# Kernel tuning notes

Measured on AMD Instinct MI355X. Metric: run time of the kernel, lower is better.

Reference implementation:

```python
import jax, jax.numpy as jnp
import numpy as np

N_NODES = 50000
N_EDGES = 1600000
NUM_GRAPHS = 64


def gcn_conv(x, edge_index, edge_weight, W, b):
    # PyG GCNConv with normalize=False: h = x @ W; out[i] = sum_{e: tgt(e)=i} w_e * h[src(e)]; out += b
    h = x @ W                                   # [N, out]
    src, tgt = edge_index[0], edge_index[1]
    msg = h[src] * edge_weight[:, None]         # [E, out] gather + scale
    out = jax.ops.segment_sum(msg, tgt, num_segments=N_NODES)
    return out + b


def setup_inputs() -> dict:
    key = jax.random.key(0)
    ks = jax.random.split(key, 10)
    x = jax.random.normal(ks[0], (N_NODES, 128), dtype=jnp.float32)
    edge_index = jax.random.randint(ks[1], (2, N_EDGES), 0, N_NODES, dtype=jnp.int64)
    edge_weight = jax.random.uniform(ks[2], (N_EDGES,), dtype=jnp.float32)
    batch = jnp.sort(jax.random.randint(ks[3], (N_NODES,), 0, NUM_GRAPHS, dtype=jnp.int64))
    W1 = jax.random.normal(ks[4], (128, 64), dtype=jnp.float32) * 0.09  # ~glorot scale
    b1 = jax.random.normal(ks[5], (64,), dtype=jnp.float32) * 0.01
    W2 = jax.random.normal(ks[6], (64, 64), dtype=jnp.float32) * 0.125
    b2 = jax.random.normal(ks[7], (64,), dtype=jnp.float32) * 0.01
    W3 = jax.random.normal(ks[8], (64, 64), dtype=jnp.float32) * 0.125
    b3 = jax.random.normal(ks[9], (64,), dtype=jnp.float32) * 0.01
    return {"x": x, "edge_index": edge_index, "edge_weight": edge_weight, "batch": batch,
            "W1": W1, "b1": b1, "W2": W2, "b2": b2, "W3": W3, "b3": b3}


def reference(x, edge_index, edge_weight, batch, W1, b1, W2, b2, W3, b3):
    # dropout is identity in eval mode
    h = jax.nn.relu(gcn_conv(x, edge_index, edge_weight, W1, b1))
    embed = gcn_conv(h, edge_index, edge_weight, W2, b2)
    graph = gcn_conv(h, edge_index, edge_weight, W3, b3)
    graph_embed = jax.ops.segment_sum(graph, batch, num_segments=NUM_GRAPHS)
    return (embed, graph_embed)
```

## Files before the change

### kernel.cpp

```cpp
#include <hip/hip_runtime.h>


typedef _Float16 f16;
typedef _Float16 h2v __attribute__((ext_vector_type(2)));

#define THREADS 256
#define BTHREADS 1024
#define NODECAP 80
#define NC 391
#define CSTRIDE 16
#define ACH 4096
#define CAPC 4736

__global__ __launch_bounds__(BTHREADS) void bin_coarse(
    const int* __restrict__ src, const int* __restrict__ tgt,
    const float* __restrict__ ew, int* __restrict__ cnt_a,
    int2* __restrict__ cbins, int E) {
  __shared__ int lcnt[NC];
  __shared__ int gbase[NC];
  int tid = threadIdx.x;
  for (int i = tid; i < NC; i += BTHREADS) lcnt[i] = 0;
  __syncthreads();

  int e0 = blockIdx.x * ACH;
  int xr[4], wr[4], cr[4];
#pragma unroll
  for (int k = 0; k < 4; ++k) {
    int e = e0 + k * BTHREADS + tid;
    if (e < E) {
      int t = tgt[e];
      int c = t >> 7;
      int r = atomicAdd(&lcnt[c], 1);
      xr[k] = (src[e] & 0xffff) | ((t & 127) << 16);
      wr[k] = __float_as_int(ew[e]);
      cr[k] = c | (r << 16);
    } else {
      cr[k] = -1;
    }
  }
  __syncthreads();

  for (int c = tid; c < NC; c += BTHREADS) {
    int n = lcnt[c];
    gbase[c] = n ? atomicAdd(&cnt_a[c * CSTRIDE], n) : 0;
  }
  __syncthreads();

#pragma unroll
  for (int k = 0; k < 4; ++k) {
    if (cr[k] < 0) continue;
    int c = cr[k] & 0xffff;
    int r = cr[k] >> 16;
    int dst = gbase[c] + r;
    if (dst < CAPC) cbins[(size_t)c * CAPC + dst] = make_int2(xr[k], wr[k]);
  }
}

__global__ __launch_bounds__(BTHREADS) void bin_fine(
    const int* __restrict__ cnt_a, const int2* __restrict__ cbins,
    int* __restrict__ cnt_f, int2* __restrict__ fbins, int N) {
  __shared__ int fcnt[128];
  int c = blockIdx.x;
  int tid = threadIdx.x;
  if (tid < 128) fcnt[tid] = 0;
  __syncthreads();
  int d = min(cnt_a[c * CSTRIDE], CAPC);
  const int2* ep = cbins + (size_t)c * CAPC;
  for (int i = tid; i < d; i += BTHREADS) {
    int2 ent = ep[i];
    int tl = ent.x >> 16;
    int r = atomicAdd(&fcnt[tl], 1);
    int node = c * 128 + tl;
    if (r < NODECAP && node < N)
      fbins[(size_t)node * NODECAP + r] = make_int2((ent.x & 0xffff) << 7, ent.y);
  }
  __syncthreads();
  if (tid < 128) {
    int node = c * 128 + tid;
    if (node < N) cnt_f[node] = min(fcnt[tid], NODECAP);
  }
}

template <bool RELU>
__global__ __launch_bounds__(THREADS) void gather_nodes(
    const f16* __restrict__ h, const int2* __restrict__ fbins,
    const int* __restrict__ cnt, const float* __restrict__ bias,
    f16* __restrict__ out, int N) {
  int tid = threadIdx.x;
  int lane = tid & 63;
  int node = blockIdx.x * 4 + (tid >> 6);
  if (node >= N) return;
  int d = min(cnt[node], NODECAP);
  const int2* ep = fbins + (size_t)node * NODECAP;
  const char* hb = (const char*)h;
  int q = lane >> 4;
  int lq = lane & 15;
  int lq8 = lq * 8;
  float4 acc = make_float4(0.f, 0.f, 0.f, 0.f);

  for (int base = 0; base < d; base += 64) {
    int take = min(64, d - base);
    int2 ent = ep[base + min(lane, take - 1)];
    int pv = ent.x;
    float wv = (lane < take) ? __int_as_float(ent.y) : 0.f;

    for (int g0 = 0; g0 < take; g0 += 32) {
      int off[8]; float w[8];
#pragma unroll
      for (int u = 0; u < 8; ++u) {
        int sl = g0 + u * 4 + q;
        off[u] = __shfl(pv, sl, 64);
        w[u]   = __shfl(wv, sl, 64);
      }
      uint2 r8[8];
#pragma unroll
      for (int u = 0; u < 8; ++u)
        r8[u] = *(const uint2*)(hb + off[u] + lq8);
#pragma unroll
      for (int u = 0; u < 8; ++u) {
        h2v p0 = __builtin_bit_cast(h2v, r8[u].x);
        h2v p1 = __builtin_bit_cast(h2v, r8[u].y);
        acc.x = fmaf((float)p0.x, w[u], acc.x);
        acc.y = fmaf((float)p0.y, w[u], acc.y);
        acc.z = fmaf((float)p1.x, w[u], acc.z);
        acc.w = fmaf((float)p1.y, w[u], acc.w);
      }
    }
  }

  acc.x += __shfl_xor(acc.x, 16, 64); acc.x += __shfl_xor(acc.x, 32, 64);
  acc.y += __shfl_xor(acc.y, 16, 64); acc.y += __shfl_xor(acc.y, 32, 64);
  acc.z += __shfl_xor(acc.z, 16, 64); acc.z += __shfl_xor(acc.z, 32, 64);
  acc.w += __shfl_xor(acc.w, 16, 64); acc.w += __shfl_xor(acc.w, 32, 64);

  if (q == 0) {
    union { f16 h4[4]; uint2 u; } pk;
    if (RELU) {
      float4 bb = *(const float4*)(bias + lq * 4);
      pk.h4[0] = (f16)fmaxf(acc.x + bb.x, 0.f);
      pk.h4[1] = (f16)fmaxf(acc.y + bb.y, 0.f);
      pk.h4[2] = (f16)fmaxf(acc.z + bb.z, 0.f);
      pk.h4[3] = (f16)fmaxf(acc.w + bb.w, 0.f);
    } else {
      pk.h4[0] = (f16)acc.x; pk.h4[1] = (f16)acc.y;
      pk.h4[2] = (f16)acc.z; pk.h4[3] = (f16)acc.w;
    }
    *(uint2*)((char*)out + (size_t)node * 128 + lq8) = pk.u;
  }
}

template <int K, bool BIAS, typename InT, typename OutT>
__global__ __launch_bounds__(THREADS) void gemm_tiled(
    const InT* __restrict__ A, const float* __restrict__ W,
    const float* __restrict__ bias, OutT* __restrict__ C, int M) {
  __shared__ float Xs[K][68];
  __shared__ float Ws[K][64];
  int tid = threadIdx.x;
  int r0 = blockIdx.x * 64;

  for (int i = tid * 4; i < K * 64; i += THREADS * 4)
    *(float4*)&Ws[0][i] = *(const float4*)(W + i);

  constexpr int KSH = (K == 128) ? 7 : 6;
  for (int i = tid * 4; i < 64 * K; i += THREADS * 4) {
    int row = i >> KSH, k = i & (K - 1);
    float4 v = make_float4(0.f, 0.f, 0.f, 0.f);
    if (r0 + row < M) {
      if constexpr (sizeof(InT) == 2) {
        uint2 u = *(const uint2*)((const f16*)A + (size_t)(r0 + row) * K + k);
        h2v a0 = __builtin_bit_cast(h2v, u.x);
        h2v a1 = __builtin_bit_cast(h2v, u.y);
        v = make_float4((float)a0.x, (float)a0.y, (float)a1.x, (float)a1.y);
      } else {
        v = *(const float4*)((const float*)A + (size_t)(r0 + row) * K + k);
      }
    }
    Xs[k + 0][row] = v.x; Xs[k + 1][row] = v.y;
    Xs[k + 2][row] = v.z; Xs[k + 3][row] = v.w;
  }
  __syncthreads();

  int tx = tid & 15, ty = tid >> 4;
  float acc[4][4] = {};
#pragma unroll 8
  for (int k = 0; k < K; ++k) {
    float4 w4 = *(const float4*)&Ws[k][tx * 4];
    float4 x4 = *(const float4*)&Xs[k][ty * 4];
    acc[0][0] = fmaf(x4.x, w4.x, acc[0][0]); acc[0][1] = fmaf(x4.x, w4.y, acc[0][1]);
    acc[0][2] = fmaf(x4.x, w4.z, acc[0][2]); acc[0][3] = fmaf(x4.x, w4.w, acc[0][3]);
    acc[1][0] = fmaf(x4.y, w4.x, acc[1][0]); acc[1][1] = fmaf(x4.y, w4.y, acc[1][1]);
    acc[1][2] = fmaf(x4.y, w4.z, acc[1][2]); acc[1][3] = fmaf(x4.y, w4.w, acc[1][3]);
    acc[2][0] = fmaf(x4.z, w4.x, acc[2][0]); acc[2][1] = fmaf(x4.z, w4.y, acc[2][1]);
    acc[2][2] = fmaf(x4.z, w4.z, acc[2][2]); acc[2][3] = fmaf(x4.z, w4.w, acc[2][3]);
    acc[3][0] = fmaf(x4.w, w4.x, acc[3][0]); acc[3][1] = fmaf(x4.w, w4.y, acc[3][1]);
    acc[3][2] = fmaf(x4.w, w4.z, acc[3][2]); acc[3][3] = fmaf(x4.w, w4.w, acc[3][3]);
  }
#pragma unroll
  for (int i = 0; i < 4; ++i) {
    int r = r0 + ty * 4 + i;
    if (r >= M) continue;
    float4 o = make_float4(acc[i][0], acc[i][1], acc[i][2], acc[i][3]);
    if (BIAS) {
      float4 bb = *(const float4*)(bias + tx * 4);
      o.x += bb.x; o.y += bb.y; o.z += bb.z; o.w += bb.w;
    }
    if constexpr (sizeof(OutT) == 2) {
      union { f16 h4[4]; uint2 u; } pk;
      pk.h4[0] = (f16)o.x; pk.h4[1] = (f16)o.y;
      pk.h4[2] = (f16)o.z; pk.h4[3] = (f16)o.w;
      *(uint2*)((f16*)C + (size_t)r * 64 + tx * 4) = pk.u;
    } else {
      *(float4*)((float*)C + (size_t)r * 64 + tx * 4) = o;
    }
  }
}

__global__ __launch_bounds__(THREADS) void graph_reduce(
    const f16* __restrict__ A, const int* __restrict__ batch,
    float* __restrict__ B, float* __restrict__ counts, int N) {
  int lane = threadIdx.x & 63;
  int chunk = blockIdx.x * (THREADS >> 6) + (threadIdx.x >> 6);
  int n0 = chunk * 64;
  if (n0 >= N) return;
  int n1 = min(n0 + 64, N);
  int cur = batch[n0];
  float acc = 0.f, cnt = 0.f;
  for (int n = n0; n < n1; ++n) {
    int g = batch[n];
    if (g != cur) {
      unsafeAtomicAdd(&B[cur * 64 + lane], acc);
      if (lane == 0) unsafeAtomicAdd(&counts[cur], cnt);
      acc = 0.f; cnt = 0.f; cur = g;
    }
    acc += (float)A[(size_t)n * 64 + lane];
    cnt += 1.f;
  }
  unsafeAtomicAdd(&B[cur * 64 + lane], acc);
  if (lane == 0) unsafeAtomicAdd(&counts[cur], cnt);
}

__global__ __launch_bounds__(THREADS) void graph_out_k(
    const float* __restrict__ B, const float* __restrict__ W3,
    const float* __restrict__ b3, const float* __restrict__ counts,
    float* __restrict__ out, int G) {
  int j = threadIdx.x & 63;
  int g = blockIdx.x * (THREADS >> 6) + (threadIdx.x >> 6);
  if (g >= G) return;
  float acc = 0.f;
#pragma unroll
  for (int k = 0; k < 64; ++k) acc += B[g * 64 + k] * W3[k * 64 + j];
  out[g * 64 + j] = acc + counts[g] * b3[j];
}

extern "C" void kernel_launch(void* const* d_in, const int* in_sizes, int n_in,
                              void* d_out, int out_size, void* d_ws, size_t ws_size,
                              hipStream_t stream) {
  const float* x     = (const float*)d_in[0];
  const int*   ei    = (const int*)d_in[1];
  const float* ew    = (const float*)d_in[2];
  const int*   batch = (const int*)d_in[3];
  const float* W1    = (const float*)d_in[4];
  const float* b1    = (const float*)d_in[5];
  const float* W2    = (const float*)d_in[6];
  const float* b2    = (const float*)d_in[7];
  const float* W3    = (const float*)d_in[8];
  const float* b3    = (const float*)d_in[9];

  const int N = in_sizes[0] / 128;
  const int E = in_sizes[1] / 2;
  const int G = (out_size - N * 64) / 64;
  const int* src = ei;
  const int* tgt = ei + E;

  float* out_embed = (float*)d_out;
  float* out_graph = (float*)d_out + (size_t)N * 64;

  char* ws = (char*)d_ws;
  f16*   hpre   = (f16*)ws;
  f16*   h1     = (f16*)(ws + (size_t)N * 64 * 2);
  f16*   A      = (f16*)(ws + (size_t)N * 64 * 4);
  int2*  cbins  = (int2*)ws;
  int*   cnt_f  = (int*)(ws + (size_t)N * 64 * 8);
  int*   cnt_a  = cnt_f + N;
  float* B      = (float*)(cnt_a + NC * CSTRIDE);
  float* counts = B + (size_t)G * 64;
  size_t meta_bytes = (size_t)(N + NC * CSTRIDE) * 4 + (size_t)(G * 64 + G) * 4;
  size_t base   = (size_t)N * 64 * 8 + meta_bytes;
  size_t fin_off = (base + 255) & ~(size_t)255;
  int2*  fbins  = (int2*)(ws + fin_off);

  hipMemsetAsync(cnt_f, 0, meta_bytes, stream);

  bin_coarse<<<(E + ACH - 1) / ACH, BTHREADS, 0, stream>>>(
      src, tgt, ew, cnt_a, cbins, E);
  bin_fine<<<NC, BTHREADS, 0, stream>>>(cnt_a, cbins, cnt_f, fbins, N);

  gemm_tiled<128, false, float, f16><<<(N + 63) / 64, THREADS, 0, stream>>>(
      x, W1, nullptr, hpre, N);

  const int gblocks = (N + 3) / 4;
  gather_nodes<true><<<gblocks, THREADS, 0, stream>>>(
      hpre, fbins, cnt_f, b1, h1, N);
  gather_nodes<false><<<gblocks, THREADS, 0, stream>>>(
      h1, fbins, cnt_f, nullptr, A, N);

  gemm_tiled<64, true, f16, float><<<(N + 63) / 64, THREADS, 0, stream>>>(
      A, W2, b2, out_embed, N);

  int chunks = (N + 63) / 64;
  graph_reduce<<<(chunks + 3) / 4, THREADS, 0, stream>>>(A, batch, B, counts, N);

  graph_out_k<<<(G + 3) / 4, THREADS, 0, stream>>>(B, W3, b3, counts, out_graph, G);
}
```

Before: 245.6 us.

## Co-schedule coarse binning with first GEMM and fuse graph reduce into second GEMM

```diff
diff --git a/kernel.cpp b/kernel.cpp
--- a/kernel.cpp
+++ b/kernel.cpp
@@ -12,21 +12,23 @@
 #define ACH 4096
 #define CAPC 4736
 
-__global__ __launch_bounds__(BTHREADS) void bin_coarse(
-    const int* __restrict__ src, const int* __restrict__ tgt,
-    const float* __restrict__ ew, int* __restrict__ cnt_a,
-    int2* __restrict__ cbins, int E) {
-  __shared__ int lcnt[NC];
-  __shared__ int gbase[NC];
-  int tid = threadIdx.x;
-  for (int i = tid; i < NC; i += BTHREADS) lcnt[i] = 0;
-  __syncthreads();
-
-  int e0 = blockIdx.x * ACH;
-  int xr[4], wr[4], cr[4];
-#pragma unroll
-  for (int k = 0; k < 4; ++k) {
-    int e = e0 + k * BTHREADS + tid;
+#define SMEM_BYTES (128 * 68 * 4 + 128 * 64 * 4)
+
+__device__ __forceinline__ void bin_coarse_body(
+    int bid, char* smem, const int* __restrict__ src,
+    const int* __restrict__ tgt, const float* __restrict__ ew,
+    int* __restrict__ cnt_a, int2* __restrict__ cbins, int E) {
+  int* lcnt  = (int*)smem;
+  int* gbase = lcnt + NC;
+  int tid = threadIdx.x;
+  for (int i = tid; i < NC; i += THREADS) lcnt[i] = 0;
+  __syncthreads();
+
+  int e0 = bid * ACH;
+  int xr[16], wr[16], cr[16];
+#pragma unroll
+  for (int k = 0; k < 16; ++k) {
+    int e = e0 + k * THREADS + tid;
     if (e < E) {
       int t = tgt[e];
       int c = t >> 7;
@@ -40,19 +42,83 @@
   }
   __syncthreads();
 
-  for (int c = tid; c < NC; c += BTHREADS) {
+  for (int c = tid; c < NC; c += THREADS) {
     int n = lcnt[c];
     gbase[c] = n ? atomicAdd(&cnt_a[c * CSTRIDE], n) : 0;
   }
   __syncthreads();
 
 #pragma unroll
-  for (int k = 0; k < 4; ++k) {
+  for (int k = 0; k < 16; ++k) {
     if (cr[k] < 0) continue;
     int c = cr[k] & 0xffff;
     int r = cr[k] >> 16;
     int dst = gbase[c] + r;
     if (dst < CAPC) cbins[(size_t)c * CAPC + dst] = make_int2(xr[k], wr[k]);
+  }
+}
+
+__device__ __forceinline__ void gemm1_body(
+    int bid, char* smem, const float* __restrict__ A,
+    const float* __restrict__ W, f16* __restrict__ C, int M) {
+  float (*Xs)[68] = (float(*)[68])smem;
+  float (*Ws)[64] = (float(*)[64])(smem + 128 * 68 * 4);
+  int tid = threadIdx.x;
+  int r0 = bid * 64;
+
+  for (int i = tid * 4; i < 128 * 64; i += THREADS * 4)
+    *(float4*)&Ws[0][i] = *(const float4*)(W + i);
+
+  for (int i = tid * 4; i < 64 * 128; i += THREADS * 4) {
+    int row = i >> 7, k = i & 127;
+    float4 v = make_float4(0.f, 0.f, 0.f, 0.f);
+    if (r0 + row < M) v = *(const float4*)(A + (size_t)(r0 + row) * 128 + k);
+    Xs[k + 0][row] = v.x; Xs[k + 1][row] = v.y;
+    Xs[k + 2][row] = v.z; Xs[k + 3][row] = v.w;
+  }
+  __syncthreads();
+
+  int tx = tid & 15, ty = tid >> 4;
+  float acc[4][4] = {};
+#pragma unroll 8
+  for (int k = 0; k < 128; ++k) {
+    float4 w4 = *(const float4*)&Ws[k][tx * 4];
+    float4 x4 = *(const float4*)&Xs[k][ty * 4];
+    acc[0][0] = fmaf(x4.x, w4.x, acc[0][0]); acc[0][1] = fmaf(x4.x, w4.y, acc[0][1]);
+    acc[0][2] = fmaf(x4.x, w4.z, acc[0][2]); acc[0][3] = fmaf(x4.x, w4.w, acc[0][3]);
+    acc[1][0] = fmaf(x4.y, w4.x, acc[1][0]); acc[1][1] = fmaf(x4.y, w4.y, acc[1][1]);
+    acc[1][2] = fmaf(x4.y, w4.z, acc[1][2]); acc[1][3] = fmaf(x4.y, w4.w, acc[1][3]);
+    acc[2][0] = fmaf(x4.z, w4.x, acc[2][0]); acc[2][1] = fmaf(x4.z, w4.y, acc[2][1]);
+    acc[2][2] = fmaf(x4.z, w4.z, acc[2][2]); acc[2][3] = fmaf(x4.z, w4.w, acc[2][3]);
+    acc[3][0] = fmaf(x4.w, w4.x, acc[3][0]); acc[3][1] = fmaf(x4.w, w4.y, acc[3][1]);
+    acc[3][2] = fmaf(x4.w, w4.z, acc[3][2]); acc[3][3] = fmaf(x4.w, w4.w, acc[3][3]);
+  }
+#pragma unroll
+  for (int i = 0; i < 4; ++i) {
+    int r = r0 + ty * 4 + i;
+    if (r >= M) continue;
+    union { f16 h4[4]; uint2 u; } pk;
+    pk.h4[0] = (f16)acc[i][0]; pk.h4[1] = (f16)acc[i][1];
+    pk.h4[2] = (f16)acc[i][2]; pk.h4[3] = (f16)acc[i][3];
+    *(uint2*)(C + (size_t)r * 64 + tx * 4) = pk.u;
+  }
+}
+
+__global__ __launch_bounds__(THREADS) void k_bin_gemm(
+    const int* __restrict__ src, const int* __restrict__ tgt,
+    const float* __restrict__ ew, int* __restrict__ cnt_a,
+    int2* __restrict__ cbins, int E,
+    const float* __restrict__ x, const float* __restrict__ W1,
+    f16* __restrict__ hpre, int M, int NBIN, int NGEMM) {
+  __shared__ __align__(16) char smem[SMEM_BYTES];
+  int b = blockIdx.x;
+  int binid = (b % 3 == 0) ? b / 3 : -1;
+  if (binid >= 0 && binid < NBIN) {
+    bin_coarse_body(binid, smem, src, tgt, ew, cnt_a, cbins, E);
+  } else {
+    int nb = min((b + 2) / 3, NBIN);
+    int gi = b - nb;
+    if (gi < NGEMM) gemm1_body(gi, smem, x, W1, hpre, M);
   }
 }
 
@@ -149,31 +215,29 @@
   }
 }
 
-template <int K, bool BIAS, typename InT, typename OutT>
-__global__ __launch_bounds__(THREADS) void gemm_tiled(
-    const InT* __restrict__ A, const float* __restrict__ W,
-    const float* __restrict__ bias, OutT* __restrict__ C, int M) {
-  __shared__ float Xs[K][68];
-  __shared__ float Ws[K][64];
+__global__ __launch_bounds__(THREADS) void k_gemm2_reduce(
+    const f16* __restrict__ A, const float* __restrict__ W,
+    const float* __restrict__ bias, const int* __restrict__ batch,
+    float* __restrict__ C, float* __restrict__ B, float* __restrict__ counts,
+    int M) {
+  __shared__ float Xs[64][68];
+  __shared__ float Ws[64][64];
+  __shared__ int bsh[64];
   int tid = threadIdx.x;
   int r0 = blockIdx.x * 64;
 
-  for (int i = tid * 4; i < K * 64; i += THREADS * 4)
+  for (int i = tid * 4; i < 64 * 64; i += THREADS * 4)
     *(float4*)&Ws[0][i] = *(const float4*)(W + i);
-
-  constexpr int KSH = (K == 128) ? 7 : 6;
-  for (int i = tid * 4; i < 64 * K; i += THREADS * 4) {
-    int row = i >> KSH, k = i & (K - 1);
+  if (tid < 64) bsh[tid] = (r0 + tid < M) ? batch[r0 + tid] : -1;
+
+  for (int i = tid * 4; i < 64 * 64; i += THREADS * 4) {
+    int row = i >> 6, k = i & 63;
     float4 v = make_float4(0.f, 0.f, 0.f, 0.f);
     if (r0 + row < M) {
-      if constexpr (sizeof(InT) == 2) {
-        uint2 u = *(const uint2*)((const f16*)A + (size_t)(r0 + row) * K + k);
-        h2v a0 = __builtin_bit_cast(h2v, u.x);
-        h2v a1 = __builtin_bit_cast(h2v, u.y);
-        v = make_float4((float)a0.x, (float)a0.y, (float)a1.x, (float)a1.y);
-      } else {
-        v = *(const float4*)((const float*)A + (size_t)(r0 + row) * K + k);
-      }
+      uint2 u = *(const uint2*)(A + (size_t)(r0 + row) * 64 + k);
+      h2v a0 = __builtin_bit_cast(h2v, u.x);
+      h2v a1 = __builtin_bit_cast(h2v, u.y);
+      v = make_float4((float)a0.x, (float)a0.y, (float)a1.x, (float)a1.y);
     }
     Xs[k + 0][row] = v.x; Xs[k + 1][row] = v.y;
     Xs[k + 2][row] = v.z; Xs[k + 3][row] = v.w;
@@ -183,7 +247,7 @@
   int tx = tid & 15, ty = tid >> 4;
   float acc[4][4] = {};
 #pragma unroll 8
-  for (int k = 0; k < K; ++k) {
+  for (int k = 0; k < 64; ++k) {
     float4 w4 = *(const float4*)&Ws[k][tx * 4];
     float4 x4 = *(const float4*)&Xs[k][ty * 4];
     acc[0][0] = fmaf(x4.x, w4.x, acc[0][0]); acc[0][1] = fmaf(x4.x, w4.y, acc[0][1]);
@@ -199,44 +263,34 @@
   for (int i = 0; i < 4; ++i) {
     int r = r0 + ty * 4 + i;
     if (r >= M) continue;
-    float4 o = make_float4(acc[i][0], acc[i][1], acc[i][2], acc[i][3]);
-    if (BIAS) {
-      float4 bb = *(const float4*)(bias + tx * 4);
-      o.x += bb.x; o.y += bb.y; o.z += bb.z; o.w += bb.w;
-    }
-    if constexpr (sizeof(OutT) == 2) {
-      union { f16 h4[4]; uint2 u; } pk;
-      pk.h4[0] = (f16)o.x; pk.h4[1] = (f16)o.y;
-      pk.h4[2] = (f16)o.z; pk.h4[3] = (f16)o.w;
-      *(uint2*)((f16*)C + (size_t)r * 64 + tx * 4) = pk.u;
-    } else {
-      *(float4*)((float*)C + (size_t)r * 64 + tx * 4) = o;
-    }
-  }
-}
-
-__global__ __launch_bounds__(THREADS) void graph_reduce(
-    const f16* __restrict__ A, const int* __restrict__ batch,
-    float* __restrict__ B, float* __restrict__ counts, int N) {
-  int lane = threadIdx.x & 63;
-  int chunk = blockIdx.x * (THREADS >> 6) + (threadIdx.x >> 6);
-  int n0 = chunk * 64;
-  if (n0 >= N) return;
-  int n1 = min(n0 + 64, N);
-  int cur = batch[n0];
-  float acc = 0.f, cnt = 0.f;
-  for (int n = n0; n < n1; ++n) {
-    int g = batch[n];
+    float4 bb = *(const float4*)(bias + tx * 4);
+    float4 o = make_float4(acc[i][0] + bb.x, acc[i][1] + bb.y,
+                           acc[i][2] + bb.z, acc[i][3] + bb.w);
+    *(float4*)(C + (size_t)r * 64 + tx * 4) = o;
+  }
+
+  int k = tid & 63, p = tid >> 6;
+  float racc = 0.f, rcnt = 0.f;
+  int cur = -1;
+#pragma unroll 4
+  for (int j = 0; j < 16; ++j) {
+    int row = p * 16 + j;
+    if (r0 + row >= M) break;
+    int g = bsh[row];
     if (g != cur) {
-      unsafeAtomicAdd(&B[cur * 64 + lane], acc);
-      if (lane == 0) unsafeAtomicAdd(&counts[cur], cnt);
-      acc = 0.f; cnt = 0.f; cur = g;
-    }
-    acc += (float)A[(size_t)n * 64 + lane];
-    cnt += 1.f;
-  }
-  unsafeAtomicAdd(&B[cur * 64 + lane], acc);
-  if (lane == 0) unsafeAtomicAdd(&counts[cur], cnt);
+      if (cur >= 0) {
+        unsafeAtomicAdd(&B[cur * 64 + k], racc);
+        if (k == 0) unsafeAtomicAdd(&counts[cur], rcnt);
+      }
+      racc = 0.f; rcnt = 0.f; cur = g;
+    }
+    racc += Xs[k][row];
+    rcnt += 1.f;
+  }
+  if (cur >= 0) {
+    unsafeAtomicAdd(&B[cur * 64 + k], racc);
+    if (k == 0) unsafeAtomicAdd(&counts[cur], rcnt);
+  }
 }
 
 __global__ __launch_bounds__(THREADS) void graph_out_k(
@@ -271,32 +325,33 @@
   const int G = (out_size - N * 64) / 64;
   const int* src = ei;
   const int* tgt = ei + E;
+  const int NBIN = (E + ACH - 1) / ACH;
+  const int NGEMM = (N + 63) / 64;
 
   float* out_embed = (float*)d_out;
   float* out_graph = (float*)d_out + (size_t)N * 64;
 
   char* ws = (char*)d_ws;
   f16*   hpre   = (f16*)ws;
-  f16*   h1     = (f16*)(ws + (size_t)N * 64 * 2);
-  f16*   A      = (f16*)(ws + (size_t)N * 64 * 4);
-  int2*  cbins  = (int2*)ws;
-  int*   cnt_f  = (int*)(ws + (size_t)N * 64 * 8);
+  f16*   h1     = hpre + (size_t)N * 64;
+  f16*   A      = h1 + (size_t)N * 64;
+  int*   cnt_f  = (int*)(A + (size_t)N * 64);
   int*   cnt_a  = cnt_f + N;
   float* B      = (float*)(cnt_a + NC * CSTRIDE);
   float* counts = B + (size_t)G * 64;
-  size_t meta_bytes = (size_t)(N + NC * CSTRIDE) * 4 + (size_t)(G * 64 + G) * 4;
-  size_t base   = (size_t)N * 64 * 8 + meta_bytes;
-  size_t fin_off = (base + 255) & ~(size_t)255;
-  int2*  fbins  = (int2*)(ws + fin_off);
-
-  hipMemsetAsync(cnt_f, 0, meta_bytes, stream);
-
-  bin_coarse<<<(E + ACH - 1) / ACH, BTHREADS, 0, stream>>>(
-      src, tgt, ew, cnt_a, cbins, E);
+  size_t zero_bytes = (size_t)NC * CSTRIDE * 4 + (size_t)(G * 64 + G) * 4;
+  size_t off = ((size_t)((char*)(counts + G) - ws) + 255) & ~(size_t)255;
+  int2*  fbins  = (int2*)(ws + off);
+  off += (size_t)N * NODECAP * 8;
+  off = (off + 255) & ~(size_t)255;
+  int2*  cbins  = (int2*)(ws + off);
+
+  hipMemsetAsync(cnt_a, 0, zero_bytes, stream);
+
+  k_bin_gemm<<<NBIN + NGEMM, THREADS, 0, stream>>>(
+      src, tgt, ew, cnt_a, cbins, E, x, W1, hpre, N, NBIN, NGEMM);
+
   bin_fine<<<NC, BTHREADS, 0, stream>>>(cnt_a, cbins, cnt_f, fbins, N);
-
-  gemm_tiled<128, false, float, f16><<<(N + 63) / 64, THREADS, 0, stream>>>(
-      x, W1, nullptr, hpre, N);
 
   const int gblocks = (N + 3) / 4;
   gather_nodes<true><<<gblocks, THREADS, 0, stream>>>(
@@ -304,11 +359,8 @@
   gather_nodes<false><<<gblocks, THREADS, 0, stream>>>(
       h1, fbins, cnt_f, nullptr, A, N);
 
-  gemm_tiled<64, true, f16, float><<<(N + 63) / 64, THREADS, 0, stream>>>(
-      A, W2, b2, out_embed, N);
-
-  int chunks = (N + 63) / 64;
-  graph_reduce<<<(chunks + 3) / 4, THREADS, 0, stream>>>(A, batch, B, counts, N);
+  k_gemm2_reduce<<<NGEMM, THREADS, 0, stream>>>(
+      A, W2, b2, batch, out_embed, B, counts, N);
 
   graph_out_k<<<(G + 3) / 4, THREADS, 0, stream>>>(B, W3, b3, counts, out_graph, G);
 }
```

New measurement: 235.0 us. 1.05x faster.
